# Optimization experiments

Measured on AMD Instinct MI355X. Metric: run time of the kernel, lower is better.

The kernel has to match this reference:

```python
import jax, jax.numpy as jnp
import numpy as np
from jax.scipy.special import logsumexp


def setup_inputs() -> dict:
    key = jax.random.key(0)
    k = jax.random.split(key, 8)
    B, T, K, L = 32, 128, 16, 16
    s = 0.05
    y_batch = jax.random.uniform(k[0], (B, T, 1, 28, 28), dtype=jnp.float32)
    enc_w1 = jax.random.normal(k[1], (400, 784), dtype=jnp.float32) * s
    enc_b1 = jnp.zeros((400,), jnp.float32)
    enc_w2 = jax.random.normal(k[2], (2 * L, 400), dtype=jnp.float32) * s
    enc_b2 = jnp.zeros((2 * L,), jnp.float32)
    dec_fc_w = jax.random.normal(k[3], (400, L + K), dtype=jnp.float32) * s
    dec_fc_b = jnp.zeros((400,), jnp.float32)
    dec_w = jax.random.normal(k[4], (784, 400), dtype=jnp.float32) * s
    dec_b = jnp.zeros((784,), jnp.float32)
    log_pi = jnp.zeros((K,), jnp.float32)
    log_A = jax.random.normal(k[5], (K, K), dtype=jnp.float32)
    log_A = log_A.at[jnp.arange(K), jnp.arange(K)].set(-1e9)  # fill_diagonal_(-1e9)
    eps = jax.random.normal(k[6], (B * T, L), dtype=jnp.float32)
    return dict(y_batch=y_batch, enc_w1=enc_w1, enc_b1=enc_b1, enc_w2=enc_w2,
                enc_b2=enc_b2, dec_fc_w=dec_fc_w, dec_fc_b=dec_fc_b, dec_w=dec_w,
                dec_b=dec_b, log_pi=log_pi, log_A=log_A, eps=eps)


def reference(y_batch, enc_w1, enc_b1, enc_w2, enc_b2, dec_fc_w, dec_fc_b,
              dec_w, dec_b, log_pi, log_A, eps):
    B, T = y_batch.shape[0], y_batch.shape[1]
    K = log_pi.shape[0]
    L = eps.shape[1]
    N = B * T
    # ---- VAE emission log-likelihoods (compute_log_bk); dropout in eval mode ----
    y_flat = y_batch.reshape(N, 784)
    h = jax.nn.relu(y_flat @ enc_w1.T + enc_b1)                 # [N,400]
    ml = h @ enc_w2.T + enc_b2                                   # [N,2L]
    mu, logvar = ml[:, :L], ml[:, L:]
    z = mu + eps * jnp.exp(0.5 * logvar)                         # reparameterize
    # decode(z, one_hot(k)) for all k at once: split cat-linear into z part + k column
    Wz, Wx = dec_fc_w[:, :L], dec_fc_w[:, L:]                    # [400,L],[400,K]
    base = z @ Wz.T + dec_fc_b                                   # [N,400]
    hk = jax.nn.relu(base[None, :, :] + Wx.T[:, None, :])        # [K,N,400]
    y_rec = jax.nn.sigmoid(jnp.einsum('knh,oh->kno', hk, dec_w) + dec_b)  # [K,N,784]
    # binary_cross_entropy with torch's log clamp at -100
    logp = jnp.clip(jnp.log(y_rec), -100.0, None)
    log1mp = jnp.clip(jnp.log(1.0 - y_rec), -100.0, None)
    bce = -(y_flat[None] * logp + (1.0 - y_flat[None]) * log1mp)  # [K,N,784]
    recon = bce.sum(-1) / 100.0                                   # [K,N]
    log_bk = (-recon).reshape(K, B, T).transpose(1, 2, 0)         # [B,T,K]
    # ---- forward-backward in log domain ----
    lp = jnp.log(jax.nn.softmax(log_pi) + 1e-9)
    lA = jnp.log(jax.nn.softmax(log_A, axis=1) + 1e-9)
    lb_rest = jnp.moveaxis(log_bk[:, 1:], 1, 0)                   # [T-1,B,K]
    a0 = lp + log_bk[:, 0]                                        # [B,K]

    def fstep(prev, lb_t):
        cur = logsumexp(prev[:, :, None] + lA[None], axis=1) + lb_t
        return cur, cur

    _, alphas = jax.lax.scan(fstep, a0, lb_rest)
    log_alpha = jnp.concatenate([a0[:, None], jnp.moveaxis(alphas, 0, 1)], axis=1)  # [B,T,K]

    bT = jnp.zeros((B, K), log_bk.dtype)

    def bstep(nxt, lb_t1):
        cur = logsumexp(lA[None] + (lb_t1 + nxt)[:, None, :], axis=2)
        return cur, cur

    _, betas = jax.lax.scan(bstep, bT, lb_rest, reverse=True)     # betas[t] = beta_t, t=0..T-2
    log_beta = jnp.concatenate([jnp.moveaxis(betas, 0, 1), bT[:, None]], axis=1)  # [B,T,K]

    lg = log_alpha + log_beta
    log_gamma = lg - logsumexp(lg, axis=2, keepdims=True)

    lxi = (log_alpha[:, :-1, :, None] + lA[None, None]
           + (log_bk[:, 1:] + log_beta[:, 1:])[:, :, None, :])    # [B,T-1,K,K]
    lxi = lxi - logsumexp(lxi, axis=(2, 3), keepdims=True)
    return jnp.exp(log_gamma), jnp.exp(lxi)
```

## Files before the change

### kernel.cpp

```cpp
#include <hip/hip_runtime.h>
#include <math.h>


typedef _Float16 h8v __attribute__((ext_vector_type(8)));
typedef _Float16 h4v __attribute__((ext_vector_type(4)));
typedef float f16v __attribute__((ext_vector_type(16)));

__device__ __forceinline__ void gll16(const void* g, void* l) {
  __builtin_amdgcn_global_load_lds(
      (const __attribute__((address_space(1))) void*)g,
      (__attribute__((address_space(3))) void*)l, 16, 0, 0);
}

__global__ __launch_bounds__(256)
void k_prep(const float* __restrict__ dw, const float* __restrict__ ew1,
            _Float16* __restrict__ dwh, _Float16* __restrict__ w1h,
            float* __restrict__ lb) {
  int idx = blockIdx.x * 256 + threadIdx.x;
  if (idx < 65536) lb[idx] = 0.f;
  if (idx < 896 * 448) {
    int o = idx / 448, h2 = idx - o * 448;
    float v = (o < 784 && h2 < 400) ? dw[o * 400 + h2] : 0.f;
    dwh[idx] = (_Float16)v;
  } else if (idx < 896 * 448 + 512 * 800) {
    int j = idx - 896 * 448;
    int i = j / 800, kc = j - i * 800;
    float v = (i < 400 && kc < 784) ? ew1[i * 784 + kc] : 0.f;
    w1h[j] = (_Float16)v;
  }
}

#define E1ST 40
__global__ __launch_bounds__(256, 2)
void k_enc1(const float* __restrict__ y, const _Float16* __restrict__ w1h,
            const float* __restrict__ b1, float* __restrict__ hout) {
  __shared__ __align__(16) _Float16 Ah[64 * E1ST];
  __shared__ __align__(16) _Float16 Bh[128 * E1ST];
  const int tid = threadIdx.x;
  const int i0 = blockIdx.x * 128;
  const int n0 = blockIdx.y * 64;
  const int wav = tid >> 6, lane = tid & 63;
  const int wn = wav >> 1, wi = wav & 1;
  const int ln = lane & 31, kg = lane >> 5;

  f16v acc[2];
#pragma unroll
  for (int j = 0; j < 2; ++j)
#pragma unroll
    for (int r = 0; r < 16; ++r) acc[j][r] = 0.f;

  const int ar = tid >> 3, ac4 = (tid & 7) * 4;
  const int br = tid >> 2, bg = (tid & 3) * 8;

#pragma unroll 1
  for (int hc = 0; hc < 25; ++hc) {
    const int h0 = hc * 32;
    __syncthreads();
#pragma unroll
    for (int it = 0; it < 2; ++it) {
      int r = ar + 32 * it;
      float4 a = make_float4(0.f, 0.f, 0.f, 0.f);
      if (h0 + ac4 < 784) a = *(const float4*)&y[(n0 + r) * 784 + h0 + ac4];
      h4v hv;
      hv[0] = (_Float16)a.x; hv[1] = (_Float16)a.y;
      hv[2] = (_Float16)a.z; hv[3] = (_Float16)a.w;
      *(h4v*)&Ah[r * E1ST + ac4] = hv;
    }
#pragma unroll
    for (int it = 0; it < 2; ++it) {
      int r = br + 64 * it;
      *(h8v*)&Bh[r * E1ST + bg] = *(const h8v*)&w1h[(i0 + r) * 800 + h0 + bg];
    }
    __syncthreads();
#pragma unroll
    for (int kk = 0; kk < 2; ++kk) {
      const int ko = kk * 16 + kg * 8;
      h8v a  = *(const h8v*)&Ah[(wn * 32 + ln) * E1ST + ko];
      h8v b0 = *(const h8v*)&Bh[(wi * 64 + ln) * E1ST + ko];
      h8v b1 = *(const h8v*)&Bh[(wi * 64 + 32 + ln) * E1ST + ko];
      acc[0] = __builtin_amdgcn_mfma_f32_32x32x16_f16(a, b0, acc[0], 0, 0, 0);
      acc[1] = __builtin_amdgcn_mfma_f32_32x32x16_f16(a, b1, acc[1], 0, 0, 0);
    }
  }
#pragma unroll
  for (int j = 0; j < 2; ++j) {
    const int i = i0 + wi * 64 + j * 32 + ln;
    if (i < 400) {
      const float bias = b1[i];
#pragma unroll
      for (int reg = 0; reg < 16; ++reg) {
        const int row = n0 + wn * 32 + (reg & 3) + 8 * (reg >> 2) + 4 * kg;
        hout[row * 400 + i] = fmaxf(acc[j][reg] + bias, 0.f);
      }
    }
  }
}

__global__ __launch_bounds__(128, 2)
void k_enc2z(const float* __restrict__ h, const float* __restrict__ w2,
             const float* __restrict__ b2, const float* __restrict__ eps,
             float* __restrict__ z) {
  __shared__ __align__(16) float h_lds[16 * 400];
  __shared__ __align__(16) float w2_lds[32 * 404];
  __shared__ float ml_lds[16 * 32];
  const int tid = threadIdx.x;
  const int n0 = blockIdx.x * 16;
  for (int idx = tid; idx < 1600; idx += 128) {
    int r = idx / 100, c = idx - r * 100;
    *(float4*)&h_lds[r * 400 + c * 4] = *(const float4*)&h[(n0 + r) * 400 + c * 4];
  }
  for (int idx = tid; idx < 3200; idx += 128) {
    int r = idx / 100, c = idx - r * 100;
    *(float4*)&w2_lds[r * 404 + c * 4] = *(const float4*)&w2[r * 400 + c * 4];
  }
  __syncthreads();
  const int c_ = tid & 31, n4 = tid >> 5;
  float a0 = 0.f, a1 = 0.f, a2 = 0.f, a3 = 0.f;
  for (int q = 0; q < 100; ++q) {
    float4 wv = *(const float4*)&w2_lds[c_ * 404 + q * 4];
    float4 h0 = *(const float4*)&h_lds[(n4 * 4 + 0) * 400 + q * 4];
    float4 h1 = *(const float4*)&h_lds[(n4 * 4 + 1) * 400 + q * 4];
    float4 h2 = *(const float4*)&h_lds[(n4 * 4 + 2) * 400 + q * 4];
    float4 h3 = *(const float4*)&h_lds[(n4 * 4 + 3) * 400 + q * 4];
    a0 += h0.x * wv.x + h0.y * wv.y + h0.z * wv.z + h0.w * wv.w;
    a1 += h1.x * wv.x + h1.y * wv.y + h1.z * wv.z + h1.w * wv.w;
    a2 += h2.x * wv.x + h2.y * wv.y + h2.z * wv.z + h2.w * wv.w;
    a3 += h3.x * wv.x + h3.y * wv.y + h3.z * wv.z + h3.w * wv.w;
  }
  const float bb = b2[c_];
  ml_lds[(n4 * 4 + 0) * 32 + c_] = a0 + bb;
  ml_lds[(n4 * 4 + 1) * 32 + c_] = a1 + bb;
  ml_lds[(n4 * 4 + 2) * 32 + c_] = a2 + bb;
  ml_lds[(n4 * 4 + 3) * 32 + c_] = a3 + bb;
  __syncthreads();
  for (int t = tid; t < 256; t += 128) {
    int n2 = t >> 4, l = t & 15;
    float mu = ml_lds[n2 * 32 + l];
    float lv = ml_lds[n2 * 32 + 16 + l];
    z[(n0 + n2) * 16 + l] = mu + eps[(n0 + n2) * 16 + l] * expf(0.5f * lv);
  }
}

__global__ __launch_bounds__(256, 4)
void k_base(const float* __restrict__ z, const float* __restrict__ dfw,
            const float* __restrict__ dfb, float* __restrict__ basep) {
  __shared__ float z_lds[16 * 16];
  __shared__ __align__(16) float wz_lds[400 * 20];
  const int tid = threadIdx.x;
  const int n0 = blockIdx.x * 16;
  if (tid < 64) {
    int n = tid >> 2, c = (tid & 3) * 4;
    *(float4*)&z_lds[n * 16 + c] = *(const float4*)&z[(n0 + n) * 16 + c];
  }
  for (int idx = tid; idx < 1600; idx += 256) {
    int i = idx >> 2, c = (idx & 3) * 4;
    *(float4*)&wz_lds[i * 20 + c] = *(const float4*)&dfw[i * 32 + c];
  }
  __syncthreads();
  for (int idx = tid; idx < 7168; idx += 256) {
    int n = idx / 448, i = idx - n * 448;
    float acc = 0.f;
    if (i < 400) {
      acc = dfb[i];
#pragma unroll
      for (int q = 0; q < 4; ++q) {
        float4 zv = *(const float4*)&z_lds[n * 16 + q * 4];
        float4 wv = *(const float4*)&wz_lds[i * 20 + q * 4];
        acc += zv.x * wv.x + zv.y * wv.y + zv.z * wv.z + zv.w * wv.w;
      }
    }
    basep[(n0 + n) * 448 + i] = acc;
  }
}

__global__ __launch_bounds__(256, 4)
void k_hk(const float* __restrict__ basep, const float* __restrict__ dfw,
          _Float16* __restrict__ hkh) {
  __shared__ float wxT[16 * 448];
  const int tid = threadIdx.x;
  const int n0 = blockIdx.x * 8;
  for (int idx = tid; idx < 7168; idx += 256) {
    int k = idx / 448, hh = idx - k * 448;
    wxT[idx] = (hh < 400) ? dfw[hh * 32 + 16 + k] : 0.f;
  }
  __syncthreads();
  for (int s = tid; s < 448; s += 256) {
    int r = s / 56, c8 = s - r * 56;
    const float* bp = &basep[(size_t)(n0 + r) * 448 + c8 * 8];
    float4 b0 = *(const float4*)bp;
    float4 b1 = *(const float4*)(bp + 4);
#pragma unroll
    for (int k = 0; k < 16; ++k) {
      const float* wp = &wxT[k * 448 + c8 * 8];
      float4 w0 = *(const float4*)wp;
      float4 w1 = *(const float4*)(wp + 4);
      h8v o;
      o[0] = (_Float16)fmaxf(b0.x + w0.x, 0.f);
      o[1] = (_Float16)fmaxf(b0.y + w0.y, 0.f);
      o[2] = (_Float16)fmaxf(b0.z + w0.z, 0.f);
      o[3] = (_Float16)fmaxf(b0.w + w0.w, 0.f);
      o[4] = (_Float16)fmaxf(b1.x + w1.x, 0.f);
      o[5] = (_Float16)fmaxf(b1.y + w1.y, 0.f);
      o[6] = (_Float16)fmaxf(b1.z + w1.z, 0.f);
      o[7] = (_Float16)fmaxf(b1.w + w1.w, 0.f);
      *(h8v*)&hkh[((size_t)k * 4096 + n0 + r) * 448 + c8 * 8] = o;
    }
  }
}

__global__ __launch_bounds__(256, 2)
void k_dec2(const _Float16* __restrict__ hkh, const _Float16* __restrict__ dwh,
            const float* __restrict__ decb, const float* __restrict__ y,
            float* __restrict__ lb) {
  __shared__ __align__(16) _Float16 Ah[128 * 64];
  __shared__ __align__(16) _Float16 Bh[128 * 64];
  __shared__ float red[256];

  const int tid = threadIdx.x;
  const int id  = blockIdx.x;
  const int lin = (id & 7) * 448 + (id >> 3);
  const int n_i = lin / 112;
  const int rem = lin - n_i * 112;
  const int k   = rem / 7;
  const int ot  = rem - k * 7;
  const int n0  = n_i * 128;
  const int o0  = ot * 128;

  const int wav = tid >> 6, lane = tid & 63;
  const int wn = wav >> 1, wo = wav & 1;
  const int ln = lane & 31, kg = lane >> 5;

  const int l8 = lane >> 3, l7 = lane & 7;
  const int swh = (l7 * 8) ^ (l8 * 8);
  const _Float16* hkk = hkh + (size_t)k * 4096 * 448;
  const _Float16* pA[4];
  const _Float16* pB[4];
#pragma unroll
  for (int i = 0; i < 4; ++i) {
    const int row = wav * 32 + i * 8 + l8;
    pA[i] = hkk + (size_t)(n0 + row) * 448 + swh;
    pB[i] = dwh + (size_t)(o0 + row) * 448 + swh;
  }

  f16v acc[2][2];
#pragma unroll
  for (int i = 0; i < 2; ++i)
#pragma unroll
    for (int j = 0; j < 2; ++j)
#pragma unroll
      for (int r = 0; r < 16; ++r) acc[i][j][r] = 0.f;

  const int sx = (ln & 7) * 8;
  const int e0 = (kg * 8) ^ sx;
  const int arow = (wn * 64 + ln) * 64;
  const int brow = (wo * 64 + ln) * 64;

#pragma unroll 1
  for (int hc = 0; hc < 7; ++hc) {
    __syncthreads();
#pragma unroll
    for (int i = 0; i < 4; ++i) {
      gll16(pA[i], &Ah[(wav * 4 + i) * 512]);
      gll16(pB[i], &Bh[(wav * 4 + i) * 512]);
      pA[i] += 64; pB[i] += 64;
    }
    __syncthreads();
#pragma unroll
    for (int kk = 0; kk < 4; ++kk) {
      const int cx = (kk * 16) ^ e0;
      h8v a0 = *(const h8v*)&Ah[arow + cx];
      h8v a1 = *(const h8v*)&Ah[arow + 2048 + cx];
      h8v b0 = *(const h8v*)&Bh[brow + cx];
      h8v b1 = *(const h8v*)&Bh[brow + 2048 + cx];
      acc[0][0] = __builtin_amdgcn_mfma_f32_32x32x16_f16(a0, b0, acc[0][0], 0, 0, 0);
      acc[1][0] = __builtin_amdgcn_mfma_f32_32x32x16_f16(a1, b0, acc[1][0], 0, 0, 0);
      acc[0][1] = __builtin_amdgcn_mfma_f32_32x32x16_f16(a0, b1, acc[0][1], 0, 0, 0);
      acc[1][1] = __builtin_amdgcn_mfma_f32_32x32x16_f16(a1, b1, acc[1][1], 0, 0, 0);
    }
  }
  const int obase = o0 + wo * 64;
  const float bj0 = (obase + ln < 784) ? decb[obase + ln] : 0.f;
  const float bj1 = (obase + 32 + ln < 784) ? decb[obase + 32 + ln] : 0.f;
#pragma unroll
  for (int i = 0; i < 2; ++i) {
#pragma unroll
    for (int reg = 0; reg < 16; ++reg) {
      const int row = wn * 64 + i * 32 + (reg & 3) + 8 * (reg >> 2) + 4 * kg;
      float v = 0.f;
#pragma unroll
      for (int j = 0; j < 2; ++j) {
        const int o = obase + j * 32 + ln;
        if (o < 784) {
          float x = acc[i][j][reg] + (j ? bj1 : bj0);
          float yv = y[(n0 + row) * 784 + o];
          float spx = fmaxf(x, 0.f) + __logf(1.f + __expf(-fabsf(x)));
          float t2 = fminf(spx, 100.f);
          float t1 = fminf(spx - x, 100.f);
          v += t2 + yv * (t1 - t2);
        }
      }
      v += __shfl_xor(v, 1, 64);
      v += __shfl_xor(v, 2, 64);
      v += __shfl_xor(v, 4, 64);
      v += __shfl_xor(v, 8, 64);
      v += __shfl_xor(v, 16, 64);
      if (ln == 0) red[wo * 128 + row] = v;
    }
  }
  __syncthreads();
  if (tid < 128) {
    float s = red[tid] + red[128 + tid];
    atomicAdd(&lb[(n0 + tid) * 16 + k], s);
  }
}

#define DST 72
__global__ __launch_bounds__(256, 2)
void k_dec1(const float* __restrict__ basep, const float* __restrict__ dfw,
            const _Float16* __restrict__ dwh, const float* __restrict__ decb,
            const float* __restrict__ y, float* __restrict__ lb) {
  __shared__ __align__(16) _Float16 Ah[128 * DST];
  __shared__ __align__(16) _Float16 Bh[128 * DST];
  __shared__ float wx[448];
  __shared__ float red[256];

  const int tid = threadIdx.x;
  const int id  = blockIdx.x;
  const int lin = (id & 7) * 448 + (id >> 3);
  const int n_i = lin / 112;
  const int rem = lin - n_i * 112;
  const int k   = rem / 7;
  const int ot  = rem - k * 7;
  const int n0  = n_i * 128;
  const int o0  = ot * 128;
  const bool full = (ot < 6);

  const int wav = tid >> 6, lane = tid & 63;
  const int wn = wav >> 1, wo = wav & 1;
  const int ln = lane & 31, kg = lane >> 5;

  for (int i = tid; i < 448; i += 256) wx[i] = (i < 400) ? dfw[i * 32 + 16 + k] : 0.f;

  const int ar = tid >> 4, ac4 = (tid & 15) * 4;
  const int br = tid >> 3, bg = (tid & 7) * 8;
  const float* aptr = basep + (long)(n0 + ar) * 448 + ac4;

  float4 apf[8];
#pragma unroll
  for (int it = 0; it < 8; ++it) apf[it] = *(const float4*)&aptr[(16 * it) * 448];

  f16v acc[2][2];
#pragma unroll
  for (int i = 0; i < 2; ++i)
#pragma unroll
    for (int j = 0; j < 2; ++j)
#pragma unroll
      for (int r = 0; r < 16; ++r) acc[i][j][r] = 0.f;

#pragma unroll 1
  for (int hc = 0; hc < 7; ++hc) {
    const int h0 = hc * 64;
    h8v bpf[4];
#pragma unroll
    for (int it = 0; it < 4; ++it)
      bpf[it] = *(const h8v*)&dwh[(o0 + br + 32 * it) * 448 + h0 + bg];
    __syncthreads();
    {
      float4 w = *(const float4*)&wx[h0 + ac4];
#pragma unroll
      for (int it = 0; it < 8; ++it) {
        int r = ar + 16 * it;
        h4v hv;
        hv[0] = (_Float16)fmaxf(apf[it].x + w.x, 0.f);
        hv[1] = (_Float16)fmaxf(apf[it].y + w.y, 0.f);
        hv[2] = (_Float16)fmaxf(apf[it].z + w.z, 0.f);
        hv[3] = (_Float16)fmaxf(apf[it].w + w.w, 0.f);
        *(h4v*)&Ah[r * DST + ac4] = hv;
      }
    }
#pragma unroll
    for (int it = 0; it < 4; ++it)
      *(h8v*)&Bh[(br + 32 * it) * DST + bg] = bpf[it];
    __syncthreads();
    if (hc < 6) {
      const int hn = (hc + 1) * 64;
#pragma unroll
      for (int it = 0; it < 8; ++it)
        apf[it] = *(const float4*)&aptr[(16 * it) * 448 + hn];
    }
#pragma unroll
    for (int kk = 0; kk < 4; ++kk) {
      const int ko = kk * 16 + kg * 8;
      h8v a0 = *(const h8v*)&Ah[(wn * 64 + ln) * DST + ko];
      h8v a1 = *(const h8v*)&Ah[(wn * 64 + 32 + ln) * DST + ko];
      h8v b0 = *(const h8v*)&Bh[(wo * 64 + ln) * DST + ko];
      h8v b1 = *(const h8v*)&Bh[(wo * 64 + 32 + ln) * DST + ko];
      if (full) {
        acc[0][0] = __builtin_amdgcn_mfma_f32_32x32x16_f16(a0, b0, acc[0][0], 0, 0, 0);
        acc[1][0] = __builtin_amdgcn_mfma_f32_32x32x16_f16(a1, b0, acc[1][0], 0, 0, 0);
        acc[0][1] = __builtin_amdgcn_mfma_f32_32x32x16_f16(a0, b1, acc[0][1], 0, 0, 0);
        acc[1][1] = __builtin_amdgcn_mfma_f32_32x32x16_f16(a1, b1, acc[1][1], 0, 0, 0);
      } else if (wo == 0) {
        acc[0][0] = __builtin_amdgcn_mfma_f32_32x32x16_f16(a0, b0, acc[0][0], 0, 0, 0);
        acc[1][0] = __builtin_amdgcn_mfma_f32_32x32x16_f16(a1, b0, acc[1][0], 0, 0, 0);
      }
    }
  }
  const int obase = o0 + wo * 64;
  const float bj0 = (obase + ln < 784) ? decb[obase + ln] : 0.f;
  const float bj1 = (obase + 32 + ln < 784) ? decb[obase + 32 + ln] : 0.f;
#pragma unroll
  for (int i = 0; i < 2; ++i) {
#pragma unroll
    for (int reg = 0; reg < 16; ++reg) {
      const int row = wn * 64 + i * 32 + (reg & 3) + 8 * (reg >> 2) + 4 * kg;
      float v = 0.f;
#pragma unroll
      for (int j = 0; j < 2; ++j) {
        const int o = obase + j * 32 + ln;
        if (o < 784) {
          float x = acc[i][j][reg] + (j ? bj1 : bj0);
          float yv = y[(n0 + row) * 784 + o];
          float spx = fmaxf(x, 0.f) + __logf(1.f + __expf(-fabsf(x)));
          float t2 = fminf(spx, 100.f);
          float t1 = fminf(spx - x, 100.f);
          v += t2 + yv * (t1 - t2);
        }
      }
      v += __shfl_xor(v, 1, 64);
      v += __shfl_xor(v, 2, 64);
      v += __shfl_xor(v, 4, 64);
      v += __shfl_xor(v, 8, 64);
      v += __shfl_xor(v, 16, 64);
      if (ln == 0) red[wo * 128 + row] = v;
    }
  }
  __syncthreads();
  if (tid < 128) {
    float s = red[tid] + red[128 + tid];
    atomicAdd(&lb[(n0 + tid) * 16 + k], s);
  }
}

__global__ __launch_bounds__(256, 2)
void k_hmm(const float* __restrict__ lb, const float* __restrict__ lpi,
           const float* __restrict__ lA, float* __restrict__ out,
           float* __restrict__ g_ah, float* __restrict__ g_pb,
           float* __restrict__ g_sinv, float* __restrict__ g_Al) {
  __shared__ float btl[128 * 16];
  __shared__ float ah[128 * 16];
  __shared__ float bh[128 * 16];
  __shared__ float braw[128 * 16];
  __shared__ float A_l[16 * 17];
  __shared__ float pi_l[16];
  const int tid = threadIdx.x;
  const int b = blockIdx.x;

  for (int idx = tid; idx < 512; idx += 256) {
    float4 v = *(const float4*)&lb[b * 2048 + idx * 4];
    v.x *= -0.01f; v.y *= -0.01f; v.z *= -0.01f; v.w *= -0.01f;
    *(float4*)&btl[idx * 4] = v;
  }
  if (tid < 16) {
    const int j = tid;
    float m = -1e30f;
#pragma unroll
    for (int q = 0; q < 16; ++q) m = fmaxf(m, lA[j * 16 + q]);
    float e[16]; float s = 0.f;
#pragma unroll
    for (int q = 0; q < 16; ++q) { e[q] = expf(lA[j * 16 + q] - m); s += e[q]; }
    float inv = 1.f / s;
#pragma unroll
    for (int q = 0; q < 16; ++q) {
      float v = e[q] * inv + 1e-9f;
      A_l[j * 17 + q] = v;
      g_Al[j * 16 + q] = v;
    }
  } else if (tid == 16) {
    float m = -1e30f;
#pragma unroll
    for (int q = 0; q < 16; ++q) m = fmaxf(m, lpi[q]);
    float e[16]; float s = 0.f;
#pragma unroll
    for (int q = 0; q < 16; ++q) { e[q] = expf(lpi[q] - m); s += e[q]; }
    float inv = 1.f / s;
#pragma unroll
    for (int q = 0; q < 16; ++q) pi_l[q] = e[q] * inv + 1e-9f;
  }
  __syncthreads();
  if (tid < 128) {
    const int t = tid;
    float v[16]; float m = -1e30f;
#pragma unroll
    for (int q = 0; q < 16; ++q) { v[q] = btl[t * 16 + q]; m = fmaxf(m, v[q]); }
#pragma unroll
    for (int q = 0; q < 16; ++q) btl[t * 16 + q] = expf(v[q] - m);
  }
  __syncthreads();
  const int lane = tid & 63;
  const int kk = lane & 15, grp = lane >> 4;
  if (tid < 64) {
    float v0 = pi_l[kk] * btl[kk];
    float ss0 = v0;
    ss0 += __shfl_xor(ss0, 1, 64); ss0 += __shfl_xor(ss0, 2, 64);
    ss0 += __shfl_xor(ss0, 4, 64); ss0 += __shfl_xor(ss0, 8, 64);
    if (grp == 0) ah[kk] = v0 / ss0;
    for (int t = 1; t < 128; ++t) {
      float acc = 0.f;
#pragma unroll
      for (int jj = 0; jj < 4; ++jj) {
        int j = grp * 4 + jj;
        acc = fmaf(ah[(t - 1) * 16 + j], A_l[j * 17 + kk], acc);
      }
      acc += __shfl_xor(acc, 16, 64);
      acc += __shfl_xor(acc, 32, 64);
      float v = acc * btl[t * 16 + kk];
      float ss = v;
      ss += __shfl_xor(ss, 1, 64); ss += __shfl_xor(ss, 2, 64);
      ss += __shfl_xor(ss, 4, 64); ss += __shfl_xor(ss, 8, 64);
      if (grp == 0) ah[t * 16 + kk] = v / ss;
    }
  } else if (tid < 128) {
    if (grp == 0) bh[127 * 16 + kk] = 1.f;
    for (int t = 126; t >= 0; --t) {
      float acc = 0.f;
#pragma unroll
      for (int q = 0; q < 4; ++q) {
        int k2 = grp * 4 + q;
        acc = fmaf(A_l[kk * 17 + k2], btl[(t + 1) * 16 + k2] * bh[(t + 1) * 16 + k2], acc);
      }
      acc += __shfl_xor(acc, 16, 64);
      acc += __shfl_xor(acc, 32, 64);
      float ss = acc;
      ss += __shfl_xor(ss, 1, 64); ss += __shfl_xor(ss, 2, 64);
      ss += __shfl_xor(ss, 4, 64); ss += __shfl_xor(ss, 8, 64);
      if (grp == 0) { braw[t * 16 + kk] = acc; bh[t * 16 + kk] = acc / ss; }
    }
  }
  __syncthreads();
  if (tid < 128) {
    const int t = tid;
    float g[16]; float s2 = 0.f;
#pragma unroll
    for (int q = 0; q < 16; ++q) { g[q] = ah[t * 16 + q] * bh[t * 16 + q]; s2 += g[q]; }
    float inv = 1.f / s2;
#pragma unroll
    for (int c = 0; c < 4; ++c) {
      float4 o;
      o.x = g[c * 4 + 0] * inv; o.y = g[c * 4 + 1] * inv;
      o.z = g[c * 4 + 2] * inv; o.w = g[c * 4 + 3] * inv;
      *(float4*)&out[(b * 128 + t) * 16 + c * 4] = o;
      float4 av = *(float4*)&ah[t * 16 + c * 4];
      *(float4*)&g_ah[(b * 128 + t) * 16 + c * 4] = av;
      float4 p;
      p.x = btl[t * 16 + c * 4 + 0] * bh[t * 16 + c * 4 + 0];
      p.y = btl[t * 16 + c * 4 + 1] * bh[t * 16 + c * 4 + 1];
      p.z = btl[t * 16 + c * 4 + 2] * bh[t * 16 + c * 4 + 2];
      p.w = btl[t * 16 + c * 4 + 3] * bh[t * 16 + c * 4 + 3];
      *(float4*)&g_pb[(b * 128 + t) * 16 + c * 4] = p;
    }
  } else {
    const int t = tid - 128;
    if (t < 127) {
      float s2 = 0.f;
#pragma unroll
      for (int q = 0; q < 16; ++q) s2 += ah[t * 16 + q] * braw[t * 16 + q];
      g_sinv[b * 128 + t] = 1.f / s2;
    }
  }
}

__global__ __launch_bounds__(256)
void k_xi(const float* __restrict__ g_ah, const float* __restrict__ g_pb,
          const float* __restrict__ g_sinv, const float* __restrict__ g_Al,
          float* __restrict__ out) {
  const int b = blockIdx.x, t = blockIdx.y;
  const int tid = threadIdx.x;
  const int j = tid >> 4, k2 = tid & 15;
  float val = g_ah[(b * 128 + t) * 16 + j] * g_Al[j * 16 + k2] *
              g_pb[(b * 128 + t + 1) * 16 + k2] * g_sinv[b * 128 + t];
  out[65536 + (b * 127 + t) * 256 + tid] = val;
}

extern "C" void kernel_launch(void* const* d_in, const int* in_sizes, int n_in,
                              void* d_out, int out_size, void* d_ws, size_t ws_size,
                              hipStream_t stream) {
  (void)in_sizes; (void)n_in; (void)out_size;
  const float* y   = (const float*)d_in[0];
  const float* ew1 = (const float*)d_in[1];
  const float* eb1 = (const float*)d_in[2];
  const float* ew2 = (const float*)d_in[3];
  const float* eb2 = (const float*)d_in[4];
  const float* dfw = (const float*)d_in[5];
  const float* dfb = (const float*)d_in[6];
  const float* dw  = (const float*)d_in[7];
  const float* db  = (const float*)d_in[8];
  const float* lpi = (const float*)d_in[9];
  const float* lA  = (const float*)d_in[10];
  const float* eps = (const float*)d_in[11];
  float* out = (float*)d_out;

  float* ws = (float*)d_ws;
  float* h      = ws;
  float* basep  = ws;
  float* z      = ws + 1835008;
  float* lb     = z + 65536;
  _Float16* dwh = (_Float16*)(lb + 65536);
  _Float16* w1h = dwh + 896 * 448;
  float* g_ah   = (float*)(w1h + 512 * 800);
  float* g_pb   = g_ah + 65536;
  float* g_sinv = g_pb + 65536;
  float* g_Al   = g_sinv + 4096;
  _Float16* hkh = (_Float16*)(g_Al + 256);

  const bool big_ws = (ws_size >= 68748288ull);

  k_prep<<<3168, 256, 0, stream>>>(dw, ew1, dwh, w1h, lb);
  k_enc1<<<dim3(4, 64), 256, 0, stream>>>(y, w1h, eb1, h);
  k_enc2z<<<256, 128, 0, stream>>>(h, ew2, eb2, eps, z);
  k_base<<<256, 256, 0, stream>>>(z, dfw, dfb, basep);
  if (big_ws) {
    k_hk<<<512, 256, 0, stream>>>(basep, dfw, hkh);
    k_dec2<<<3584, 256, 0, stream>>>(hkh, dwh, db, y, lb);
  } else {
    k_dec1<<<3584, 256, 0, stream>>>(basep, dfw, dwh, db, y, lb);
  }
  k_hmm<<<32, 256, 0, stream>>>(lb, lpi, lA, out, g_ah, g_pb, g_sinv, g_Al);
  k_xi<<<dim3(32, 127), 256, 0, stream>>>(g_ah, g_pb, g_sinv, g_Al, out);
}
```

Measured before the change: 335.5 us.

## Double-buffer A tile in decoder GEMM and simplify BCE epilogue

Replaces the decoder GEMM main loop with a double-buffered A tile (prefetching the next hk chunk while computing on the current one), using raw s_barrier and explicit vmcnt waits instead of __syncthreads pairs. The B tile stays single-buffered and is reloaded after a barrier. The BCE epilogue drops the 100 clamps and computes softplus(x) - y*x directly. That removes a few ops but can change results when logits are extreme. The goal is to hide global-to-LDS load latency behind MFMA work, at the cost of more LDS use and more delicate synchronisation.

```diff
diff --git a/kernel.cpp b/kernel.cpp
--- a/kernel.cpp
+++ b/kernel.cpp
@@ -209,10 +209,10 @@
 }
 
 __global__ __launch_bounds__(256, 2)
-void k_dec2(const _Float16* __restrict__ hkh, const _Float16* __restrict__ dwh,
+void k_dec3(const _Float16* __restrict__ hkh, const _Float16* __restrict__ dwh,
             const float* __restrict__ decb, const float* __restrict__ y,
             float* __restrict__ lb) {
-  __shared__ __align__(16) _Float16 Ah[128 * 64];
+  __shared__ __align__(16) _Float16 AhB[2][128 * 64];
   __shared__ __align__(16) _Float16 Bh[128 * 64];
   __shared__ float red[256];
 
@@ -232,7 +232,7 @@
 
   const int l8 = lane >> 3, l7 = lane & 7;
   const int swh = (l7 * 8) ^ (l8 * 8);
-  const _Float16* hkk = hkh + (size_t)k * 4096 * 448;
+  const _Float16* hkk = hkh + (size_t)k * (4096 * 448);
   const _Float16* pA[4];
   const _Float16* pB[4];
 #pragma unroll
@@ -250,26 +250,30 @@
 #pragma unroll
       for (int r = 0; r < 16; ++r) acc[i][j][r] = 0.f;
 
+#pragma unroll
+  for (int i = 0; i < 4; ++i) { gll16(pA[i], &AhB[0][(wav * 4 + i) * 512]); pA[i] += 64; }
+#pragma unroll
+  for (int i = 0; i < 4; ++i) { gll16(pB[i], &Bh[(wav * 4 + i) * 512]);     pB[i] += 64; }
+#pragma unroll
+  for (int i = 0; i < 4; ++i) { gll16(pA[i], &AhB[1][(wav * 4 + i) * 512]); pA[i] += 64; }
+  asm volatile("s_waitcnt vmcnt(4)" ::: "memory");
+  __builtin_amdgcn_sched_barrier(0);
+  __builtin_amdgcn_s_barrier();
+
   const int sx = (ln & 7) * 8;
   const int e0 = (kg * 8) ^ sx;
   const int arow = (wn * 64 + ln) * 64;
   const int brow = (wo * 64 + ln) * 64;
 
+  int cur = 0;
 #pragma unroll 1
   for (int hc = 0; hc < 7; ++hc) {
-    __syncthreads();
-#pragma unroll
-    for (int i = 0; i < 4; ++i) {
-      gll16(pA[i], &Ah[(wav * 4 + i) * 512]);
-      gll16(pB[i], &Bh[(wav * 4 + i) * 512]);
-      pA[i] += 64; pB[i] += 64;
-    }
-    __syncthreads();
+    const _Float16* Ac = AhB[cur];
 #pragma unroll
     for (int kk = 0; kk < 4; ++kk) {
       const int cx = (kk * 16) ^ e0;
-      h8v a0 = *(const h8v*)&Ah[arow + cx];
-      h8v a1 = *(const h8v*)&Ah[arow + 2048 + cx];
+      h8v a0 = *(const h8v*)&Ac[arow + cx];
+      h8v a1 = *(const h8v*)&Ac[arow + 2048 + cx];
       h8v b0 = *(const h8v*)&Bh[brow + cx];
       h8v b1 = *(const h8v*)&Bh[brow + 2048 + cx];
       acc[0][0] = __builtin_amdgcn_mfma_f32_32x32x16_f16(a0, b0, acc[0][0], 0, 0, 0);
@@ -277,7 +281,22 @@
       acc[0][1] = __builtin_amdgcn_mfma_f32_32x32x16_f16(a0, b1, acc[0][1], 0, 0, 0);
       acc[1][1] = __builtin_amdgcn_mfma_f32_32x32x16_f16(a1, b1, acc[1][1], 0, 0, 0);
     }
-  }
+    if (hc == 6) break;
+    __builtin_amdgcn_s_barrier();
+#pragma unroll
+    for (int i = 0; i < 4; ++i) { gll16(pB[i], &Bh[(wav * 4 + i) * 512]); pB[i] += 64; }
+    if (hc < 5) {
+#pragma unroll
+      for (int i = 0; i < 4; ++i) { gll16(pA[i], &AhB[cur][(wav * 4 + i) * 512]); pA[i] += 64; }
+      asm volatile("s_waitcnt vmcnt(4)" ::: "memory");
+    } else {
+      asm volatile("s_waitcnt vmcnt(0)" ::: "memory");
+    }
+    __builtin_amdgcn_sched_barrier(0);
+    __builtin_amdgcn_s_barrier();
+    cur ^= 1;
+  }
+
   const int obase = o0 + wo * 64;
   const float bj0 = (obase + ln < 784) ? decb[obase + ln] : 0.f;
   const float bj1 = (obase + 32 + ln < 784) ? decb[obase + 32 + ln] : 0.f;
@@ -294,9 +313,7 @@
           float x = acc[i][j][reg] + (j ? bj1 : bj0);
           float yv = y[(n0 + row) * 784 + o];
           float spx = fmaxf(x, 0.f) + __logf(1.f + __expf(-fabsf(x)));
-          float t2 = fminf(spx, 100.f);
-          float t1 = fminf(spx - x, 100.f);
-          v += t2 + yv * (t1 - t2);
+          v += spx - yv * x;
         }
       }
       v += __shfl_xor(v, 1, 64);
@@ -621,7 +638,7 @@
   k_base<<<256, 256, 0, stream>>>(z, dfw, dfb, basep);
   if (big_ws) {
     k_hk<<<512, 256, 0, stream>>>(basep, dfw, hkh);
-    k_dec2<<<3584, 256, 0, stream>>>(hkh, dwh, db, y, lb);
+    k_dec3<<<3584, 256, 0, stream>>>(hkh, dwh, db, y, lb);
   } else {
     k_dec1<<<3584, 256, 0, stream>>>(basep, dfw, dwh, db, y, lb);
   }
```

Result: slower. 364.0 us (+8.5%).

## Fuse base and hk kernels; shrink decoder GEMM tile to 128x64 output

Applied to the files above, without the earlier changes.

Merges k_base and k_hk into one kernel that keeps the base activations in LDS, so the fp32 basep round trip through global memory and one launch go away. The decoder GEMM kernel now uses 128x64 tiles (13 output tiles instead of 7) with one B fragment per wave and two MFMA accumulators. The padded output columns are trimmed from 896 to 832, and lower register use allows 4 blocks per CU. The per-block LDS reduction is replaced by direct atomicAdds per row, and the BCE clamp at 100 is simplified to spx - y*x. This adds more atomics and re-reads the A tile more often, and dropping the clamp may change results slightly for extreme logits.

```diff
diff --git a/kernel.cpp b/kernel.cpp
--- a/kernel.cpp
+++ b/kernel.cpp
@@ -141,6 +141,63 @@
   }
 }
 
+__global__ __launch_bounds__(256, 2)
+void k_basehk(const float* __restrict__ z, const float* __restrict__ dfw,
+              const float* __restrict__ dfb, _Float16* __restrict__ hkh) {
+  __shared__ float z_lds[16 * 16];
+  __shared__ __align__(16) float wz[400 * 20];
+  __shared__ __align__(16) float base[16 * 448];
+  const int tid = threadIdx.x;
+  const int n0 = blockIdx.x * 16;
+  if (tid < 64) {
+    int n = tid >> 2, c = (tid & 3) * 4;
+    *(float4*)&z_lds[n * 16 + c] = *(const float4*)&z[(n0 + n) * 16 + c];
+  }
+  for (int idx = tid; idx < 1600; idx += 256) {
+    int i = idx >> 2, c = (idx & 3) * 4;
+    *(float4*)&wz[i * 20 + c] = *(const float4*)&dfw[i * 32 + c];
+  }
+  __syncthreads();
+  for (int idx = tid; idx < 7168; idx += 256) {
+    int n = idx / 448, i = idx - n * 448;
+    float acc = 0.f;
+    if (i < 400) {
+      acc = dfb[i];
+#pragma unroll
+      for (int q = 0; q < 4; ++q) {
+        float4 zv = *(const float4*)&z_lds[n * 16 + q * 4];
+        float4 wv = *(const float4*)&wz[i * 20 + q * 4];
+        acc += zv.x * wv.x + zv.y * wv.y + zv.z * wv.z + zv.w * wv.w;
+      }
+    }
+    base[n * 448 + i] = acc;
+  }
+  __syncthreads();
+  for (int idx = tid; idx < 7168; idx += 256) {
+    int k = idx / 448, hh = idx - k * 448;
+    wz[idx] = (hh < 400) ? dfw[hh * 32 + 16 + k] : 0.f;
+  }
+  __syncthreads();
+  for (int s = tid; s < 14336; s += 256) {
+    int k = s / 896, r2 = s - k * 896;
+    int r = r2 / 56, c8 = r2 - r * 56;
+    const float* bp = &base[r * 448 + c8 * 8];
+    const float* wp = &wz[k * 448 + c8 * 8];
+    float4 b0 = *(const float4*)bp, b1 = *(const float4*)(bp + 4);
+    float4 w0 = *(const float4*)wp, w1 = *(const float4*)(wp + 4);
+    h8v o;
+    o[0] = (_Float16)fmaxf(b0.x + w0.x, 0.f);
+    o[1] = (_Float16)fmaxf(b0.y + w0.y, 0.f);
+    o[2] = (_Float16)fmaxf(b0.z + w0.z, 0.f);
+    o[3] = (_Float16)fmaxf(b0.w + w0.w, 0.f);
+    o[4] = (_Float16)fmaxf(b1.x + w1.x, 0.f);
+    o[5] = (_Float16)fmaxf(b1.y + w1.y, 0.f);
+    o[6] = (_Float16)fmaxf(b1.z + w1.z, 0.f);
+    o[7] = (_Float16)fmaxf(b1.w + w1.w, 0.f);
+    *(h8v*)&hkh[((size_t)k * 4096 + n0 + r) * 448 + c8 * 8] = o;
+  }
+}
+
 __global__ __launch_bounds__(256, 4)
 void k_base(const float* __restrict__ z, const float* __restrict__ dfw,
             const float* __restrict__ dfb, float* __restrict__ basep) {
@@ -174,57 +231,21 @@
 }
 
 __global__ __launch_bounds__(256, 4)
-void k_hk(const float* __restrict__ basep, const float* __restrict__ dfw,
-          _Float16* __restrict__ hkh) {
-  __shared__ float wxT[16 * 448];
-  const int tid = threadIdx.x;
-  const int n0 = blockIdx.x * 8;
-  for (int idx = tid; idx < 7168; idx += 256) {
-    int k = idx / 448, hh = idx - k * 448;
-    wxT[idx] = (hh < 400) ? dfw[hh * 32 + 16 + k] : 0.f;
-  }
-  __syncthreads();
-  for (int s = tid; s < 448; s += 256) {
-    int r = s / 56, c8 = s - r * 56;
-    const float* bp = &basep[(size_t)(n0 + r) * 448 + c8 * 8];
-    float4 b0 = *(const float4*)bp;
-    float4 b1 = *(const float4*)(bp + 4);
-#pragma unroll
-    for (int k = 0; k < 16; ++k) {
-      const float* wp = &wxT[k * 448 + c8 * 8];
-      float4 w0 = *(const float4*)wp;
-      float4 w1 = *(const float4*)(wp + 4);
-      h8v o;
-      o[0] = (_Float16)fmaxf(b0.x + w0.x, 0.f);
-      o[1] = (_Float16)fmaxf(b0.y + w0.y, 0.f);
-      o[2] = (_Float16)fmaxf(b0.z + w0.z, 0.f);
-      o[3] = (_Float16)fmaxf(b0.w + w0.w, 0.f);
-      o[4] = (_Float16)fmaxf(b1.x + w1.x, 0.f);
-      o[5] = (_Float16)fmaxf(b1.y + w1.y, 0.f);
-      o[6] = (_Float16)fmaxf(b1.z + w1.z, 0.f);
-      o[7] = (_Float16)fmaxf(b1.w + w1.w, 0.f);
-      *(h8v*)&hkh[((size_t)k * 4096 + n0 + r) * 448 + c8 * 8] = o;
-    }
-  }
-}
-
-__global__ __launch_bounds__(256, 2)
-void k_dec2(const _Float16* __restrict__ hkh, const _Float16* __restrict__ dwh,
+void k_dec4(const _Float16* __restrict__ hkh, const _Float16* __restrict__ dwh,
             const float* __restrict__ decb, const float* __restrict__ y,
             float* __restrict__ lb) {
   __shared__ __align__(16) _Float16 Ah[128 * 64];
-  __shared__ __align__(16) _Float16 Bh[128 * 64];
-  __shared__ float red[256];
+  __shared__ __align__(16) _Float16 Bh[64 * 64];
 
   const int tid = threadIdx.x;
   const int id  = blockIdx.x;
-  const int lin = (id & 7) * 448 + (id >> 3);
-  const int n_i = lin / 112;
-  const int rem = lin - n_i * 112;
-  const int k   = rem / 7;
-  const int ot  = rem - k * 7;
+  const int lin = (id & 7) * 832 + (id >> 3);
+  const int n_i = lin / 208;
+  const int rem = lin - n_i * 208;
+  const int k   = rem / 13;
+  const int ot  = rem - k * 13;
   const int n0  = n_i * 128;
-  const int o0  = ot * 128;
+  const int o0  = ot * 64;
 
   const int wav = tid >> 6, lane = tid & 63;
   const int wn = wav >> 1, wo = wav & 1;
@@ -232,85 +253,67 @@
 
   const int l8 = lane >> 3, l7 = lane & 7;
   const int swh = (l7 * 8) ^ (l8 * 8);
-  const _Float16* hkk = hkh + (size_t)k * 4096 * 448;
+  const _Float16* hkk = hkh + (size_t)k * (4096 * 448);
   const _Float16* pA[4];
-  const _Float16* pB[4];
-#pragma unroll
-  for (int i = 0; i < 4; ++i) {
-    const int row = wav * 32 + i * 8 + l8;
-    pA[i] = hkk + (size_t)(n0 + row) * 448 + swh;
-    pB[i] = dwh + (size_t)(o0 + row) * 448 + swh;
-  }
-
-  f16v acc[2][2];
+  const _Float16* pB[2];
+#pragma unroll
+  for (int i = 0; i < 4; ++i)
+    pA[i] = hkk + (size_t)(n0 + wav * 32 + i * 8 + l8) * 448 + swh;
 #pragma unroll
   for (int i = 0; i < 2; ++i)
-#pragma unroll
-    for (int j = 0; j < 2; ++j)
-#pragma unroll
-      for (int r = 0; r < 16; ++r) acc[i][j][r] = 0.f;
-
-  const int sx = (ln & 7) * 8;
-  const int e0 = (kg * 8) ^ sx;
+    pB[i] = dwh + (size_t)(o0 + wav * 16 + i * 8 + l8) * 448 + swh;
+
+  f16v acc[2];
+#pragma unroll
+  for (int i = 0; i < 2; ++i)
+#pragma unroll
+    for (int r = 0; r < 16; ++r) acc[i][r] = 0.f;
+
+  const int e0 = (kg * 8) ^ ((ln & 7) * 8);
   const int arow = (wn * 64 + ln) * 64;
-  const int brow = (wo * 64 + ln) * 64;
+  const int brow = (wo * 32 + ln) * 64;
 
 #pragma unroll 1
   for (int hc = 0; hc < 7; ++hc) {
     __syncthreads();
 #pragma unroll
-    for (int i = 0; i < 4; ++i) {
-      gll16(pA[i], &Ah[(wav * 4 + i) * 512]);
-      gll16(pB[i], &Bh[(wav * 4 + i) * 512]);
-      pA[i] += 64; pB[i] += 64;
-    }
+    for (int i = 0; i < 4; ++i) { gll16(pA[i], &Ah[(wav * 4 + i) * 512]); pA[i] += 64; }
+#pragma unroll
+    for (int i = 0; i < 2; ++i) { gll16(pB[i], &Bh[(wav * 2 + i) * 512]); pB[i] += 64; }
     __syncthreads();
 #pragma unroll
     for (int kk = 0; kk < 4; ++kk) {
       const int cx = (kk * 16) ^ e0;
       h8v a0 = *(const h8v*)&Ah[arow + cx];
       h8v a1 = *(const h8v*)&Ah[arow + 2048 + cx];
-      h8v b0 = *(const h8v*)&Bh[brow + cx];
-      h8v b1 = *(const h8v*)&Bh[brow + 2048 + cx];
-      acc[0][0] = __builtin_amdgcn_mfma_f32_32x32x16_f16(a0, b0, acc[0][0], 0, 0, 0);
-      acc[1][0] = __builtin_amdgcn_mfma_f32_32x32x16_f16(a1, b0, acc[1][0], 0, 0, 0);
-      acc[0][1] = __builtin_amdgcn_mfma_f32_32x32x16_f16(a0, b1, acc[0][1], 0, 0, 0);
-      acc[1][1] = __builtin_amdgcn_mfma_f32_32x32x16_f16(a1, b1, acc[1][1], 0, 0, 0);
-    }
-  }
-  const int obase = o0 + wo * 64;
-  const float bj0 = (obase + ln < 784) ? decb[obase + ln] : 0.f;
-  const float bj1 = (obase + 32 + ln < 784) ? decb[obase + 32 + ln] : 0.f;
+      h8v b  = *(const h8v*)&Bh[brow + cx];
+      acc[0] = __builtin_amdgcn_mfma_f32_32x32x16_f16(a0, b, acc[0], 0, 0, 0);
+      acc[1] = __builtin_amdgcn_mfma_f32_32x32x16_f16(a1, b, acc[1], 0, 0, 0);
+    }
+  }
+
+  const int o = o0 + wo * 32 + ln;
+  const bool ov = (o < 784);
+  const float bj = ov ? decb[o] : 0.f;
 #pragma unroll
   for (int i = 0; i < 2; ++i) {
 #pragma unroll
     for (int reg = 0; reg < 16; ++reg) {
       const int row = wn * 64 + i * 32 + (reg & 3) + 8 * (reg >> 2) + 4 * kg;
       float v = 0.f;
-#pragma unroll
-      for (int j = 0; j < 2; ++j) {
-        const int o = obase + j * 32 + ln;
-        if (o < 784) {
-          float x = acc[i][j][reg] + (j ? bj1 : bj0);
-          float yv = y[(n0 + row) * 784 + o];
-          float spx = fmaxf(x, 0.f) + __logf(1.f + __expf(-fabsf(x)));
-          float t2 = fminf(spx, 100.f);
-          float t1 = fminf(spx - x, 100.f);
-          v += t2 + yv * (t1 - t2);
-        }
+      if (ov) {
+        float x = acc[i][reg] + bj;
+        float yv = y[(n0 + row) * 784 + o];
+        float spx = fmaxf(x, 0.f) + __logf(1.f + __expf(-fabsf(x)));
+        v = spx - yv * x;
       }
       v += __shfl_xor(v, 1, 64);
       v += __shfl_xor(v, 2, 64);
       v += __shfl_xor(v, 4, 64);
       v += __shfl_xor(v, 8, 64);
       v += __shfl_xor(v, 16, 64);
-      if (ln == 0) red[wo * 128 + row] = v;
-    }
-  }
-  __syncthreads();
-  if (tid < 128) {
-    float s = red[tid] + red[128 + tid];
-    atomicAdd(&lb[(n0 + tid) * 16 + k], s);
+      if (ln == 0) atomicAdd(&lb[(n0 + row) * 16 + k], v);
+    }
   }
 }
 
@@ -618,11 +621,11 @@
   k_prep<<<3168, 256, 0, stream>>>(dw, ew1, dwh, w1h, lb);
   k_enc1<<<dim3(4, 64), 256, 0, stream>>>(y, w1h, eb1, h);
   k_enc2z<<<256, 128, 0, stream>>>(h, ew2, eb2, eps, z);
-  k_base<<<256, 256, 0, stream>>>(z, dfw, dfb, basep);
   if (big_ws) {
-    k_hk<<<512, 256, 0, stream>>>(basep, dfw, hkh);
-    k_dec2<<<3584, 256, 0, stream>>>(hkh, dwh, db, y, lb);
+    k_basehk<<<256, 256, 0, stream>>>(z, dfw, dfb, hkh);
+    k_dec4<<<6656, 256, 0, stream>>>(hkh, dwh, db, y, lb);
   } else {
+    k_base<<<256, 256, 0, stream>>>(z, dfw, dfb, basep);
     k_dec1<<<3584, 256, 0, stream>>>(basep, dfw, dwh, db, y, lb);
   }
   k_hmm<<<32, 256, 0, stream>>>(lb, lpi, lA, out, g_ah, g_pb, g_sinv, g_Al);
```

Result: slower. 611.4 us (+82.2%).
